# Optimization experiments

Hardware: AMD Instinct MI355X
Metric: run time of the kernel (lower is better)

## Reference

```python
import jax, jax.numpy as jnp
import numpy as np

T, B, I, H = 1024, 64, 512, 512


def setup_inputs() -> dict:
    key = jax.random.key(0)
    ks = jax.random.split(key, 7)
    s = 1.0 / np.sqrt(H).astype(np.float32)
    return {
        "x": jax.random.normal(ks[0], (T, B, I), dtype=jnp.float32),
        "h0": jax.random.normal(ks[1], (B, H), dtype=jnp.float32),
        "c0": jax.random.normal(ks[2], (B, H), dtype=jnp.float32),
        "W_ih": jax.random.normal(ks[3], (4 * H, I), dtype=jnp.float32) * s,
        "W_hh": jax.random.normal(ks[4], (4 * H, H), dtype=jnp.float32) * s,
        "b_ih": jax.random.normal(ks[5], (4 * H,), dtype=jnp.float32) * s,
        "b_hh": jax.random.normal(ks[6], (4 * H,), dtype=jnp.float32) * s,
        "alpha": jnp.ones((1,), dtype=jnp.float32),
    }


def reference(x, h0, c0, W_ih, W_hh, b_ih, b_hh, alpha):
    # Precompute input-to-hidden projections for all timesteps in one GEMM.
    # x: [T, B, I] -> xg: [T, B, 4H]
    xg = jnp.einsum("tbi,gi->tbg", x, W_ih) + b_ih
    a = alpha[0]

    def step(carry, xg_t):
        h, c = carry  # [B, H] each
        gates = xg_t + h @ W_hh.T + b_hh  # [B, 4H]
        i, f, g, o = jnp.split(gates, 4, axis=-1)
        i = jax.nn.sigmoid(i)
        f = jax.nn.sigmoid(f)
        g = jnp.tanh(g)
        o = jax.nn.sigmoid(o)
        c_new = f * c + i * g
        h_new = o * jnp.tanh(c_new)
        # alpha step-size interpolation (alpha=1 -> plain LSTM)
        c_out = a * c_new + (1.0 - a) * c
        h_out = a * h_new + (1.0 - a) * h
        return (h_out, c_out), h_out

    (hT, cT), ys = jax.lax.scan(step, (h0, c0), xg)
    return ys, hT, cT
```

## Files before the change

kernel.cpp:

```cpp
#include <hip/hip_runtime.h>

typedef __attribute__((ext_vector_type(8))) short short8;
typedef __attribute__((ext_vector_type(4))) float f32x4;
typedef __attribute__((ext_vector_type(4))) float float4v;
typedef __attribute__((ext_vector_type(4))) unsigned short u16x4;
typedef __attribute__((ext_vector_type(4))) unsigned int u32x4;

#define T_TOT   1024
#define BATCH   64
#define HID     512
#define G4      2048
#define NGRID   128
#define BH      (BATCH * HID)

static __device__ __forceinline__ unsigned short f2bf(float x) {
  union { float f; unsigned u; } v; v.f = x;
  unsigned r = v.u + 0x7FFFu + ((v.u >> 16) & 1u);
  return (unsigned short)(r >> 16);
}
static __device__ __forceinline__ float sigm(float x) {
  return 1.0f / (1.0f + __expf(-x));
}
static __device__ __forceinline__ float tanh_fast(float x) {
  return 1.0f - 2.0f / (__expf(2.0f * x) + 1.0f);
}
static __device__ __forceinline__ void bar_lds() {
  asm volatile("s_waitcnt lgkmcnt(0)" ::: "memory");
  __builtin_amdgcn_s_barrier();
  asm volatile("" ::: "memory");
}

__global__ void init_k(const float* __restrict__ h0, const float* __restrict__ c0,
                       unsigned int* __restrict__ hb2, float* __restrict__ cst,
                       float* __restrict__ hst) {
  const int i = blockIdx.x * 256 + threadIdx.x;
  if (i < BH) {
    const float h = h0[i];
    hb2[i] = (unsigned)f2bf(h);
    hb2[BH + i] = 0xFFFF0000u;
    hst[i] = h;
    cst[i] = c0[i];
  }
}

__global__ __launch_bounds__(256) void xz_gemm(
    const float* __restrict__ A, const float* __restrict__ W,
    const float* __restrict__ bih, const float* __restrict__ bhh,
    float* __restrict__ xzp) {
  __shared__ unsigned short As[128 * 64];
  __shared__ unsigned short Bs[128 * 64];
  const int tid  = threadIdx.x;
  const int lane = tid & 63;
  const int wid  = tid >> 6;
  const int wm   = (wid >> 1) * 64;
  const int wn   = (wid & 1) * 64;
  const int l15  = lane & 15;
  const int l4   = lane >> 4;
  const long bm  = blockIdx.x;
  const long bn  = blockIdx.y;

  f32x4 acc[4][4];
#pragma unroll
  for (int mt = 0; mt < 4; ++mt)
#pragma unroll
    for (int nt = 0; nt < 4; ++nt) acc[mt][nt] = f32x4{0.f, 0.f, 0.f, 0.f};

  const float* Ab = A + bm * 128 * 512;
  const float* Wb = W + bn * 128 * 512;
  const int r0 = tid >> 4;
  const int cq = (tid & 15) * 4;

  for (int k0 = 0; k0 < 512; k0 += 64) {
#pragma unroll
    for (int pass = 0; pass < 8; ++pass) {
      const int r = pass * 16 + r0;
      const float4v va = *(const float4v*)(Ab + (long)r * 512 + k0 + cq);
      const float4v vb = *(const float4v*)(Wb + (long)r * 512 + k0 + cq);
      u16x4 pa, pb;
#pragma unroll
      for (int j = 0; j < 4; ++j) { pa[j] = f2bf(va[j]); pb[j] = f2bf(vb[j]); }
      const int boff = r * 128 + ((cq * 2) ^ ((r & 7) << 4));
      *(u16x4*)((char*)As + boff) = pa;
      *(u16x4*)((char*)Bs + boff) = pb;
    }
    __syncthreads();
#pragma unroll
    for (int kk = 0; kk < 2; ++kk) {
      short8 af[4], bfv[4];
#pragma unroll
      for (int mt = 0; mt < 4; ++mt) {
        const int row = wm + mt * 16 + l15;
        af[mt] = *(const short8*)((const char*)As + row * 128 +
                                  ((kk * 64 + l4 * 16) ^ ((row & 7) << 4)));
      }
#pragma unroll
      for (int nt = 0; nt < 4; ++nt) {
        const int row = wn + nt * 16 + l15;
        bfv[nt] = *(const short8*)((const char*)Bs + row * 128 +
                                   ((kk * 64 + l4 * 16) ^ ((row & 7) << 4)));
      }
#pragma unroll
      for (int mt = 0; mt < 4; ++mt)
#pragma unroll
        for (int nt = 0; nt < 4; ++nt)
          acc[mt][nt] = __builtin_amdgcn_mfma_f32_16x16x32_bf16(af[mt], bfv[nt], acc[mt][nt], 0, 0, 0);
    }
    __syncthreads();
  }

#pragma unroll
  for (int nt = 0; nt < 4; ++nt) {
    const int gn = (int)(bn * 128) + wn + nt * 16 + l15;
    const float bias = bih[gn] + bhh[gn];
    const int g2  = gn >> 9;
    const int hh  = gn & 511;
    const int nb2 = hh >> 4;
    const int en2 = hh & 15;
#pragma unroll
    for (int mt = 0; mt < 4; ++mt) {
      const int m0 = (int)(bm * 128) + wm + mt * 16 + l4 * 4;
#pragma unroll
      for (int r = 0; r < 4; ++r) {
        const int m = m0 + r;
        const int tt2 = m >> 6, brow = m & 63;
        const int mb2 = brow >> 4, em2 = brow & 15;
        xzp[((((size_t)tt2 * 4 + mb2) * 32 + nb2) << 10) + em2 * 64 + g2 * 16 + en2] =
            acc[mt][nt][r] + bias;
      }
    }
  }
}

__global__ __launch_bounds__(256, 1) void lstm_steps(
    const float* __restrict__ xzp,
    const float* __restrict__ Whh,
    const float* __restrict__ alpha_p,
    float* __restrict__ out,
    unsigned int* __restrict__ hb2,
    float* __restrict__ cst, float* __restrict__ hst,
    int t0, int Tc) {
  const int bx  = blockIdx.x;
  const int mb  = bx >> 5;
  const int nb  = bx & 31;
  const int rb0 = mb * 16;
  const int hs0 = nb * 16;
  const int tid = threadIdx.x;
  const int lane = tid & 63;
  const int w   = tid >> 6;
  const int l15 = lane & 15;
  const int l4  = lane >> 4;

  __shared__ __align__(16) unsigned short h_lds[16 * HID];
  __shared__ __align__(16) float gates[4][16][20];

  short8 wf[16];
  {
    const float* wr = Whh + (long)(w * HID + hs0 + l15) * HID + l4 * 8;
#pragma unroll
    for (int ks = 0; ks < 16; ++ks) {
      const float4v lo = *(const float4v*)(wr + ks * 32);
      const float4v hi = *(const float4v*)(wr + ks * 32 + 4);
      short8 f;
#pragma unroll
      for (int j = 0; j < 4; ++j) {
        f[j]     = (short)f2bf(lo[j]);
        f[j + 4] = (short)f2bf(hi[j]);
      }
      wf[ks] = f;
    }
  }
  const float a = alpha_p[0];
  const float oma = 1.0f - a;

  const int em = tid >> 4;
  const int en = tid & 15;
  float cp = cst[(long)(rb0 + em) * HID + hs0 + en];
  float hp = hst[(long)(rb0 + em) * HID + hs0 + en];

  const long YS = (long)T_TOT * BATCH * HID;

  float xz0, xz1, xz2, xz3;
  u32x4 sa[4], sb[4];
  {
    const float* xb = xzp + (((size_t)0 * 4 + mb) * 32 + nb) * 1024 + w * 16 + l15;
    asm volatile("global_load_dword %0, %1, off" : "=v"(xz0) : "v"(xb + (l4 * 4 + 0) * 64));
    asm volatile("global_load_dword %0, %1, off" : "=v"(xz1) : "v"(xb + (l4 * 4 + 1) * 64));
    asm volatile("global_load_dword %0, %1, off" : "=v"(xz2) : "v"(xb + (l4 * 4 + 2) * 64));
    asm volatile("global_load_dword %0, %1, off" : "=v"(xz3) : "v"(xb + (l4 * 4 + 3) * 64));
    const unsigned int* p0 = hb2 + (size_t)(t0 & 1) * BH + (size_t)(rb0 + w) * HID + lane * 8;
#pragma unroll
    for (int i = 0; i < 4; ++i) {
      const unsigned int* p = p0 + (size_t)i * 4 * HID;
      asm volatile("global_load_dwordx4 %0, %1, off sc0 sc1" : "=v"(sa[i]) : "v"(p));
      asm volatile("global_load_dwordx4 %0, %1, off sc0 sc1" : "=v"(sb[i]) : "v"(p + 4));
    }
  }

  for (int tt = 0; tt < Tc; ++tt) {
    const int t = t0 + tt;

    if (tt == 0) asm volatile("s_waitcnt vmcnt(0)" ::: "memory");
    else         asm volatile("s_waitcnt vmcnt(1)" ::: "memory");
    __builtin_amdgcn_sched_barrier(0);

    {
      const unsigned wantHi = ((unsigned)t) << 16;
      const unsigned int* p0 = hb2 + (size_t)(t & 1) * BH +
                               (size_t)(rb0 + w) * HID + lane * 8;
      for (;;) {
        unsigned bad = 0u;
#pragma unroll
        for (int i = 0; i < 4; ++i) {
          unsigned d = 0u;
#pragma unroll
          for (int j = 0; j < 4; ++j)
            d |= ((sa[i][j] ^ wantHi) | (sb[i][j] ^ wantHi));
          if (d & 0xFFFF0000u) bad |= (1u << i);
        }
        if (!__any(bad != 0u)) break;
#pragma unroll
        for (int i = 0; i < 4; ++i)
          if (bad & (1u << i)) {
            const unsigned int* p = p0 + (size_t)i * 4 * HID;
            asm volatile("global_load_dwordx4 %0, %1, off sc0 sc1" : "=v"(sa[i]) : "v"(p));
            asm volatile("global_load_dwordx4 %0, %1, off sc0 sc1" : "=v"(sb[i]) : "v"(p + 4));
          }
        asm volatile("s_waitcnt vmcnt(0)" ::: "memory");
        __builtin_amdgcn_sched_barrier(0);
      }
    }

#pragma unroll
    for (int i = 0; i < 4; ++i) {
      u32x4 pk;
      pk[0] = __builtin_amdgcn_perm(sa[i][1], sa[i][0], 0x05040100u);
      pk[1] = __builtin_amdgcn_perm(sa[i][3], sa[i][2], 0x05040100u);
      pk[2] = __builtin_amdgcn_perm(sb[i][1], sb[i][0], 0x05040100u);
      pk[3] = __builtin_amdgcn_perm(sb[i][3], sb[i][2], 0x05040100u);
      const int r = 4 * i + w;
      const int c = lane;
      *(u32x4*)((char*)h_lds + c * 256 + ((r ^ (c & 15)) << 4)) = pk;
    }
    bar_lds();

    f32x4 acc[4];
    acc[0][0] = xz0; acc[0][1] = xz1; acc[0][2] = xz2; acc[0][3] = xz3;
    acc[1] = f32x4{0.f, 0.f, 0.f, 0.f};
    acc[2] = acc[1];
    acc[3] = acc[1];
#pragma unroll
    for (int ks = 0; ks < 16; ++ks) {
      const int c = ks * 4 + l4;
      const short8 af = *(const short8*)((const char*)h_lds + c * 256 +
                                         ((l15 ^ (c & 15)) << 4));
      acc[ks & 3] = __builtin_amdgcn_mfma_f32_16x16x32_bf16(af, wf[ks], acc[ks & 3], 0, 0, 0);
    }
    {
      const f32x4 s = (acc[0] + acc[1]) + (acc[2] + acc[3]);
#pragma unroll
      for (int r = 0; r < 4; ++r)
        gates[w][l4 * 4 + r][l15] = s[r];
    }
    bar_lds();

    const float gi = gates[0][em][en], gf = gates[1][em][en];
    const float gg = gates[2][em][en], go = gates[3][em][en];
    const float ii = sigm(gi), ff = sigm(gf), oo = sigm(go);
    const float g  = tanh_fast(gg);
    const float cn = ff * cp + ii * g;
    const float hn = oo * tanh_fast(cn);
    const float co = a * cn + oma * cp;
    const float ho = a * hn + oma * hp;
    cp = co;
    hp = ho;

    {
      unsigned int* dst = hb2 + (size_t)((t + 1) & 1) * BH +
                          (long)(rb0 + em) * HID + hs0 + en;
      const unsigned w32 = (((unsigned)(t + 1)) << 16) | (unsigned)f2bf(ho);
      asm volatile("global_store_dword %0, %1, off sc0 sc1"
                   :: "v"((const void*)dst), "v"(w32) : "memory");
    }

    if (tt < Tc - 1) {
      const float* xb = xzp + (((size_t)(tt + 1) * 4 + mb) * 32 + nb) * 1024 +
                        w * 16 + l15;
      asm volatile("global_load_dword %0, %1, off" : "=v"(xz0) : "v"(xb + (l4 * 4 + 0) * 64));
      asm volatile("global_load_dword %0, %1, off" : "=v"(xz1) : "v"(xb + (l4 * 4 + 1) * 64));
      asm volatile("global_load_dword %0, %1, off" : "=v"(xz2) : "v"(xb + (l4 * 4 + 2) * 64));
      asm volatile("global_load_dword %0, %1, off" : "=v"(xz3) : "v"(xb + (l4 * 4 + 3) * 64));
      const unsigned int* pn = hb2 + (size_t)((t + 1) & 1) * BH +
                               (size_t)(rb0 + w) * HID + lane * 8;
#pragma unroll
      for (int i = 0; i < 4; ++i) {
        const unsigned int* p = pn + (size_t)i * 4 * HID;
        asm volatile("global_load_dwordx4 %0, %1, off sc0 sc1" : "=v"(sa[i]) : "v"(p));
        asm volatile("global_load_dwordx4 %0, %1, off sc0 sc1" : "=v"(sb[i]) : "v"(p + 4));
      }
      const float* op = out + ((long)t * BATCH + rb0 + em) * HID + hs0 + en;
      asm volatile("global_store_dword %0, %1, off"
                   :: "v"((const void*)op), "v"(ho) : "memory");
    }
  }

  {
    const int tl = t0 + Tc - 1;
    out[((long)tl * BATCH + rb0 + em) * HID + hs0 + en] = hp;
    if (t0 + Tc == T_TOT) {
      out[YS + (long)(rb0 + em) * HID + hs0 + en] = hp;
      out[YS + BATCH * HID + (long)(rb0 + em) * HID + hs0 + en] = cp;
    }
    cst[(long)(rb0 + em) * HID + hs0 + en] = cp;
    hst[(long)(rb0 + em) * HID + hs0 + en] = hp;
  }
}

extern "C" void kernel_launch(void* const* d_in, const int* in_sizes, int n_in,
                              void* d_out, int out_size, void* d_ws, size_t ws_size,
                              hipStream_t stream) {
  const float* x     = (const float*)d_in[0];
  const float* h0    = (const float*)d_in[1];
  const float* c0    = (const float*)d_in[2];
  const float* W_ih  = (const float*)d_in[3];
  const float* W_hh  = (const float*)d_in[4];
  const float* b_ih  = (const float*)d_in[5];
  const float* b_hh  = (const float*)d_in[6];
  const float* alpha = (const float*)d_in[7];
  float* out = (float*)d_out;

  char* ws = (char*)d_ws;
  unsigned int* hb2 = (unsigned int*)(ws + 0);
  float* cst = (float*)(ws + 262144);
  float* hst = (float*)(ws + 393216);
  float* xzp = (float*)(ws + 524288);

  int Tc = T_TOT;
  while ((size_t)Tc * 524288ull + 524288ull > ws_size && Tc > 2) Tc >>= 1;

  init_k<<<128, 256, 0, stream>>>(h0, c0, hb2, cst, hst);
  for (int t0 = 0; t0 < T_TOT; t0 += Tc) {
    dim3 gg(Tc / 2, 16);
    xz_gemm<<<gg, 256, 0, stream>>>(x + (size_t)t0 * BATCH * 512,
                                    W_ih, b_ih, b_hh, xzp);
    lstm_steps<<<NGRID, 256, 0, stream>>>(xzp, W_hh, alpha, out, hb2,
                                          cst, hst, t0, Tc);
  }
}
```

Baseline: 2.947 ms.

## Overlap next chunk's input GEMM with current chunk's recurrent LSTM steps

Splits the timeline into chunks of 128 steps and launches a fused kernel per chunk. The first 128 blocks run the sequential LSTM recurrence, and the extra blocks compute the input projection GEMM for the next chunk into a double-buffered workspace. The aim is to hide the GEMM behind the latency-bound recurrence, which uses only 128 blocks. The risk is that the GEMM blocks compete for CUs and memory bandwidth with the persistent recurrent blocks, which spin on a global flag. It also adds launches compared with a single large chunk.

```diff
diff --git a/kernel.cpp b/kernel.cpp
--- a/kernel.cpp
+++ b/kernel.cpp
@@ -43,8 +43,8 @@
   }
 }
 
-__global__ __launch_bounds__(256) void xz_gemm(
-    const float* __restrict__ A, const float* __restrict__ W,
+static __device__ __forceinline__ void gemm_body(
+    int bm, int bn, const float* __restrict__ A, const float* __restrict__ W,
     const float* __restrict__ bih, const float* __restrict__ bhh,
     float* __restrict__ xzp) {
   __shared__ unsigned short As[128 * 64];
@@ -56,8 +56,6 @@
   const int wn   = (wid & 1) * 64;
   const int l15  = lane & 15;
   const int l4   = lane >> 4;
-  const long bm  = blockIdx.x;
-  const long bn  = blockIdx.y;
 
   f32x4 acc[4][4];
 #pragma unroll
@@ -65,8 +63,8 @@
 #pragma unroll
     for (int nt = 0; nt < 4; ++nt) acc[mt][nt] = f32x4{0.f, 0.f, 0.f, 0.f};
 
-  const float* Ab = A + bm * 128 * 512;
-  const float* Wb = W + bn * 128 * 512;
+  const float* Ab = A + (long)bm * 128 * 512;
+  const float* Wb = W + (long)bn * 128 * 512;
   const int r0 = tid >> 4;
   const int cq = (tid & 15) * 4;
 
@@ -110,7 +108,7 @@
 
 #pragma unroll
   for (int nt = 0; nt < 4; ++nt) {
-    const int gn = (int)(bn * 128) + wn + nt * 16 + l15;
+    const int gn = bn * 128 + wn + nt * 16 + l15;
     const float bias = bih[gn] + bhh[gn];
     const int g2  = gn >> 9;
     const int hh  = gn & 511;
@@ -118,7 +116,7 @@
     const int en2 = hh & 15;
 #pragma unroll
     for (int mt = 0; mt < 4; ++mt) {
-      const int m0 = (int)(bm * 128) + wm + mt * 16 + l4 * 4;
+      const int m0 = bm * 128 + wm + mt * 16 + l4 * 4;
 #pragma unroll
       for (int r = 0; r < 4; ++r) {
         const int m = m0 + r;
@@ -131,15 +129,32 @@
   }
 }
 
-__global__ __launch_bounds__(256, 1) void lstm_steps(
-    const float* __restrict__ xzp,
+__global__ __launch_bounds__(256) void xz_gemm(
+    const float* __restrict__ A, const float* __restrict__ W,
+    const float* __restrict__ bih, const float* __restrict__ bhh,
+    float* __restrict__ xzp) {
+  gemm_body(blockIdx.x, blockIdx.y, A, W, bih, bhh, xzp);
+}
+
+__global__ __launch_bounds__(256, 1) void fused_chunk(
+    const float* __restrict__ xnext,
+    const float* __restrict__ Wih,
+    const float* __restrict__ bih, const float* __restrict__ bhh,
+    float* __restrict__ xzp_next,
+    const float* __restrict__ xzp_cur,
     const float* __restrict__ Whh,
     const float* __restrict__ alpha_p,
     float* __restrict__ out,
     unsigned int* __restrict__ hb2,
     float* __restrict__ cst, float* __restrict__ hst,
     int t0, int Tc) {
-  const int bx  = blockIdx.x;
+  const int bx = blockIdx.x;
+  if (bx >= NGRID) {
+    const int g = bx - NGRID;
+    gemm_body(g >> 4, g & 15, xnext, Wih, bih, bhh, xzp_next);
+    return;
+  }
+
   const int mb  = bx >> 5;
   const int nb  = bx & 31;
   const int rb0 = mb * 16;
@@ -182,7 +197,7 @@
   float xz0, xz1, xz2, xz3;
   u32x4 sa[4], sb[4];
   {
-    const float* xb = xzp + (((size_t)0 * 4 + mb) * 32 + nb) * 1024 + w * 16 + l15;
+    const float* xb = xzp_cur + (((size_t)0 * 4 + mb) * 32 + nb) * 1024 + w * 16 + l15;
     asm volatile("global_load_dword %0, %1, off" : "=v"(xz0) : "v"(xb + (l4 * 4 + 0) * 64));
     asm volatile("global_load_dword %0, %1, off" : "=v"(xz1) : "v"(xb + (l4 * 4 + 1) * 64));
     asm volatile("global_load_dword %0, %1, off" : "=v"(xz2) : "v"(xb + (l4 * 4 + 2) * 64));
@@ -283,7 +298,7 @@
     }
 
     if (tt < Tc - 1) {
-      const float* xb = xzp + (((size_t)(tt + 1) * 4 + mb) * 32 + nb) * 1024 +
+      const float* xb = xzp_cur + (((size_t)(tt + 1) * 4 + mb) * 32 + nb) * 1024 +
                         w * 16 + l15;
       asm volatile("global_load_dword %0, %1, off" : "=v"(xz0) : "v"(xb + (l4 * 4 + 0) * 64));
       asm volatile("global_load_dword %0, %1, off" : "=v"(xz1) : "v"(xb + (l4 * 4 + 1) * 64));
@@ -328,21 +343,31 @@
   const float* alpha = (const float*)d_in[7];
   float* out = (float*)d_out;
 
+  int Tc = 128;
+  while ((size_t)2 * (size_t)Tc * 524288ull + 786432ull > ws_size && Tc > 2) Tc >>= 1;
+
   char* ws = (char*)d_ws;
   unsigned int* hb2 = (unsigned int*)(ws + 0);
   float* cst = (float*)(ws + 262144);
   float* hst = (float*)(ws + 393216);
-  float* xzp = (float*)(ws + 524288);
-
-  int Tc = T_TOT;
-  while ((size_t)Tc * 524288ull + 524288ull > ws_size && Tc > 2) Tc >>= 1;
+  float* xzp0 = (float*)(ws + 786432);
+  float* xzp1 = (float*)(ws + 786432 + (size_t)Tc * 524288ull);
+  float* xzp[2] = {xzp0, xzp1};
+
+  const int nchunk = T_TOT / Tc;
+  const size_t xoff = (size_t)Tc * BATCH * 512;
+  const int nG = (Tc / 2) * 16;
 
   init_k<<<128, 256, 0, stream>>>(h0, c0, hb2, cst, hst);
-  for (int t0 = 0; t0 < T_TOT; t0 += Tc) {
+  {
     dim3 gg(Tc / 2, 16);
-    xz_gemm<<<gg, 256, 0, stream>>>(x + (size_t)t0 * BATCH * 512,
-                                    W_ih, b_ih, b_hh, xzp);
-    lstm_steps<<<NGRID, 256, 0, stream>>>(xzp, W_hh, alpha, out, hb2,
-                                          cst, hst, t0, Tc);
-  }
-}
+    xz_gemm<<<gg, 256, 0, stream>>>(x, W_ih, b_ih, b_hh, xzp[0]);
+  }
+  for (int k = 0; k < nchunk; ++k) {
+    const bool last = (k == nchunk - 1);
+    const int grid = NGRID + (last ? 0 : nG);
+    fused_chunk<<<grid, 256, 0, stream>>>(
+        x + (size_t)(k + 1) * xoff, W_ih, b_ih, b_hh, xzp[(k + 1) & 1],
+        xzp[k & 1], W_hh, alpha, out, hb2, cst, hst, k * Tc, Tc);
+  }
+}
```

Measured after the change: 2.547 ms. -13.6%, faster.
